# Performance work log

Hardware: AMD Instinct MI355X
Metric: run time of the kernel (lower is better)

Reference implementation:

```python
import jax, jax.numpy as jnp
import numpy as np

N_NODES = 100000
N_EDGES = 1600000
IN_C, HID_C, OUT_C = 128, 256, 256


def sage_conv(x, src, dst, W_l, b_l, W_r, n_nodes):
    # mean aggregation of source-node features onto destination nodes
    msg_sum = jax.ops.segment_sum(x[src], dst, num_segments=n_nodes)  # [N, F]
    deg = jax.ops.segment_sum(jnp.ones_like(dst, dtype=x.dtype), dst, num_segments=n_nodes)
    aggr = msg_sum / jnp.maximum(deg, 1.0)[:, None]
    # PyG SAGEConv: lin_l(aggr) (with bias) + lin_r(x) (no bias)
    return aggr @ W_l + b_l + x @ W_r


def setup_inputs() -> dict:
    key = jax.random.key(0)
    ks = jax.random.split(key, 12)
    x = jax.random.normal(ks[0], (N_NODES, IN_C), dtype=jnp.float32)
    edge_src = jax.random.randint(ks[1], (N_EDGES,), 0, N_NODES)
    edge_dst = jax.random.randint(ks[2], (N_EDGES,), 0, N_NODES)

    def glorot(k, fan_in, fan_out):
        s = jnp.sqrt(2.0 / (fan_in + fan_out)).astype(jnp.float32)
        return jax.random.normal(k, (fan_in, fan_out), dtype=jnp.float32) * s

    return {
        "x": x,
        "W_l0": glorot(ks[3], IN_C, HID_C), "b_l0": jnp.zeros((HID_C,), jnp.float32),
        "W_r0": glorot(ks[4], IN_C, HID_C),
        "W_l1": glorot(ks[5], HID_C, HID_C), "b_l1": jnp.zeros((HID_C,), jnp.float32),
        "W_r1": glorot(ks[6], HID_C, HID_C),
        "W_l2": glorot(ks[7], HID_C, OUT_C), "b_l2": jnp.zeros((OUT_C,), jnp.float32),
        "W_r2": glorot(ks[8], HID_C, OUT_C),
        "edge_src": edge_src,
        "edge_dst": edge_dst,
    }


def reference(x, W_l0, b_l0, W_r0, W_l1, b_l1, W_r1, W_l2, b_l2, W_r2, edge_src, edge_dst):
    n = x.shape[0]
    h = sage_conv(x, edge_src, edge_dst, W_l0, b_l0, W_r0, n)
    h = jax.nn.relu(h)  # dropout p=0.0 -> identity
    h = sage_conv(h, edge_src, edge_dst, W_l1, b_l1, W_r1, n)
    h = jax.nn.relu(h)
    h = sage_conv(h, edge_src, edge_dst, W_l2, b_l2, W_r2, n)
    return h
```

## Files before the change

### kernel.cpp

```cpp
#include <hip/hip_runtime.h>
#include <cstdint>
#include <cstddef>


#define N_NODES 100000
#define N_EDGES 1600000

#define SCAN_BLOCKS 256
#define SCAN_T 256
#define FILL_PASSES 4

typedef unsigned short ushort;
typedef unsigned int uint;
typedef __attribute__((ext_vector_type(8))) short short8;
typedef __attribute__((ext_vector_type(4))) float floatx4;

#define AS1 __attribute__((address_space(1)))
#define AS3 __attribute__((address_space(3)))

__device__ __forceinline__ float bf2f(ushort h) {
    union { uint u; float f; } c; c.u = ((uint)h) << 16; return c.f;
}
__device__ __forceinline__ ushort f2bf(float f) {
    union { float f; uint u; } c; c.f = f;
    uint u = c.u;
    return (ushort)((u + 0x7FFFu + ((u >> 16) & 1u)) >> 16);
}


__global__ void count_edges(const int* __restrict__ dst, int* __restrict__ cnt) {
    int i = blockIdx.x * blockDim.x + threadIdx.x;
    if (i < N_EDGES) atomicAdd(&cnt[dst[i]], 1);
}

__global__ __launch_bounds__(SCAN_T) void scan_partial(
    const int* __restrict__ cnt, int* __restrict__ bsum, int n)
{
    int chunk = (n + SCAN_BLOCKS - 1) / SCAN_BLOCKS;
    int beg = blockIdx.x * chunk;
    int end = beg + chunk; if (end > n) end = n;
    int t = threadIdx.x;
    int s = 0;
    for (int i = beg + t; i < end; i += SCAN_T) s += cnt[i];
    __shared__ int sh[SCAN_T];
    sh[t] = s;
    __syncthreads();
    for (int off = SCAN_T / 2; off > 0; off >>= 1) {
        if (t < off) sh[t] += sh[t + off];
        __syncthreads();
    }
    if (t == 0) bsum[blockIdx.x] = sh[0];
}

__global__ __launch_bounds__(SCAN_T) void scan_block_sums(int* __restrict__ bsum) {
    int t = threadIdx.x;
    __shared__ int sh[SCAN_T];
    int v = bsum[t];
    sh[t] = v;
    __syncthreads();
    for (int off = 1; off < SCAN_T; off <<= 1) {
        int u = (t >= off) ? sh[t - off] : 0;
        __syncthreads();
        sh[t] += u;
        __syncthreads();
    }
    bsum[t] = sh[t] - v;
}

__global__ __launch_bounds__(SCAN_T) void scan_fill(
    int* __restrict__ cnt, const int* __restrict__ bsum,
    int* __restrict__ row_ptr, int n)
{
    int chunk = (n + SCAN_BLOCKS - 1) / SCAN_BLOCKS;
    int beg = blockIdx.x * chunk;
    int end = beg + chunk; if (end > n) end = n;
    int t = threadIdx.x;
    int per = (chunk + SCAN_T - 1) / SCAN_T;
    int tb = beg + t * per;
    int te = tb + per; if (te > end) te = end;
    int s = 0;
    for (int i = tb; i < te; ++i) s += cnt[i];
    __shared__ int sh[SCAN_T];
    sh[t] = s;
    __syncthreads();
    for (int off = 1; off < SCAN_T; off <<= 1) {
        int u = (t >= off) ? sh[t - off] : 0;
        __syncthreads();
        sh[t] += u;
        __syncthreads();
    }
    int running = bsum[blockIdx.x] + sh[t] - s;
    for (int i = tb; i < te; ++i) {
        int c = cnt[i];
        row_ptr[i] = running;
        cnt[i] = running;
        running += c;
    }
    if (blockIdx.x == 0 && t == 0) row_ptr[n] = N_EDGES;
}

__global__ void fill_csr(const int* __restrict__ src, const int* __restrict__ dst,
                         int* __restrict__ cursor, int* __restrict__ col_idx) {
    int i = blockIdx.x * blockDim.x + threadIdx.x;
    if (i >= N_EDGES) return;
    int lo = (int)blockIdx.y * (N_NODES / FILL_PASSES);
    int hi = lo + (N_NODES / FILL_PASSES);
    int d = dst[i];
    if (d >= lo && d < hi) {
        int p = atomicAdd(&cursor[d], 1);
        col_idx[p] = src[i];
    }
}


__global__ void convert_x_bf16(const float* __restrict__ x, ushort* __restrict__ xb, int n4) {
    int i = blockIdx.x * blockDim.x + threadIdx.x;
    if (i >= n4) return;
    float4 v = *(const float4*)&x[(size_t)i * 4];
    ushort4 o;
    o.x = f2bf(v.x); o.y = f2bf(v.y); o.z = f2bf(v.z); o.w = f2bf(v.w);
    *(ushort4*)&xb[(size_t)i * 4] = o;
}

__global__ void transpose_w_bf16(const float* __restrict__ W, ushort* __restrict__ Wt, int kshift) {
    int i = blockIdx.x * blockDim.x + threadIdx.x;
    int K = 1 << kshift;
    if (i >= 256 * K) return;
    int n = i >> kshift;
    int k = i & (K - 1);
    Wt[i] = f2bf(W[k * 256 + n]);
}

__global__ __launch_bounds__(64) void aggregate_bf16(
    const ushort* __restrict__ xb, const int* __restrict__ row_ptr,
    const int* __restrict__ col_idx, ushort* __restrict__ outb, int F)
{
    int node = blockIdx.x;
    int t = threadIdx.x;
    int b = row_ptr[node], e = row_ptr[node + 1];
    float d = (float)(e - b); if (d < 1.f) d = 1.f;
    float inv = 1.f / d;

    if (F == 256) {
        int c = t * 4;
        float a0 = 0.f, a1 = 0.f, a2 = 0.f, a3 = 0.f;
        float b0 = 0.f, b1 = 0.f, b2 = 0.f, b3 = 0.f;
        int i = b;
        for (; i + 1 < e; i += 2) {
            int s0 = col_idx[i];
            int s1 = col_idx[i + 1];
            uint2 v0 = *(const uint2*)&xb[(size_t)s0 * 256 + c];
            uint2 v1 = *(const uint2*)&xb[(size_t)s1 * 256 + c];
            a0 += bf2f((ushort)(v0.x & 0xffff)); a1 += bf2f((ushort)(v0.x >> 16));
            a2 += bf2f((ushort)(v0.y & 0xffff)); a3 += bf2f((ushort)(v0.y >> 16));
            b0 += bf2f((ushort)(v1.x & 0xffff)); b1 += bf2f((ushort)(v1.x >> 16));
            b2 += bf2f((ushort)(v1.y & 0xffff)); b3 += bf2f((ushort)(v1.y >> 16));
        }
        if (i < e) {
            int s0 = col_idx[i];
            uint2 v0 = *(const uint2*)&xb[(size_t)s0 * 256 + c];
            a0 += bf2f((ushort)(v0.x & 0xffff)); a1 += bf2f((ushort)(v0.x >> 16));
            a2 += bf2f((ushort)(v0.y & 0xffff)); a3 += bf2f((ushort)(v0.y >> 16));
        }
        ushort4 o;
        o.x = f2bf((a0 + b0) * inv); o.y = f2bf((a1 + b1) * inv);
        o.z = f2bf((a2 + b2) * inv); o.w = f2bf((a3 + b3) * inv);
        *(ushort4*)&outb[(size_t)node * 256 + c] = o;
    } else {
        int c = t * 2;
        float a0 = 0.f, a1 = 0.f, b0 = 0.f, b1 = 0.f;
        int i = b;
        for (; i + 1 < e; i += 2) {
            int s0 = col_idx[i];
            int s1 = col_idx[i + 1];
            uint v0 = *(const uint*)&xb[(size_t)s0 * 128 + c];
            uint v1 = *(const uint*)&xb[(size_t)s1 * 128 + c];
            a0 += bf2f((ushort)(v0 & 0xffff)); a1 += bf2f((ushort)(v0 >> 16));
            b0 += bf2f((ushort)(v1 & 0xffff)); b1 += bf2f((ushort)(v1 >> 16));
        }
        if (i < e) {
            int s0 = col_idx[i];
            uint v0 = *(const uint*)&xb[(size_t)s0 * 128 + c];
            a0 += bf2f((ushort)(v0 & 0xffff)); a1 += bf2f((ushort)(v0 >> 16));
        }
        ushort2 o;
        o.x = f2bf((a0 + b0) * inv); o.y = f2bf((a1 + b1) * inv);
        *(ushort2*)&outb[(size_t)node * 128 + c] = o;
    }
}

__global__ __launch_bounds__(512, 4) void gemm_wres(
    const ushort* __restrict__ A1, const ushort* __restrict__ W1t,
    const ushort* __restrict__ A2, const ushort* __restrict__ W2t,
    const float* __restrict__ bias, ushort* __restrict__ out_bf,
    float* __restrict__ out_f32, int M, int K, int relu)
{
    __shared__ __align__(16) ushort Wl[32 * 128 * 8];
    int tid = threadIdx.x;
    int w = tid >> 6, lane = tid & 63;
    int m_ = lane & 15, koq = lane >> 4;
    int c0 = blockIdx.y * 128;
    int row0 = blockIdx.x * 256;
    int KQ = K >> 3;
    int nj = (KQ * 128) >> 9;
    int nk = K >> 5;

    floatx4 acc[2][8];
#pragma unroll
    for (int i = 0; i < 2; ++i)
#pragma unroll
        for (int f = 0; f < 8; ++f) acc[i][f] = (floatx4){0.f, 0.f, 0.f, 0.f};

    int ra = row0 + w * 32 + m_;      if (ra > M - 1) ra = M - 1;
    int rb = row0 + w * 32 + 16 + m_; if (rb > M - 1) rb = M - 1;

    for (int mm = 0; mm < 2; ++mm) {
        const ushort* __restrict__ A  = mm ? A2 : A1;
        const ushort* __restrict__ Wt = mm ? W2t : W1t;
        if (mm) __syncthreads();
        for (int j = 0; j < nj; ++j) {
            int s = j * 512 + tid;
            int q = s >> 7, col = s & 127;
            __builtin_amdgcn_global_load_lds(
                (const AS1 uint*)&Wt[(size_t)(c0 + col) * K + q * 8],
                (AS3 uint*)&Wl[(size_t)(j * 512 + w * 64) * 8], 16, 0, 0);
        }
        __syncthreads();

        const ushort* __restrict__ Aa = &A[(size_t)ra * K + koq * 8];
        const ushort* __restrict__ Ab = &A[(size_t)rb * K + koq * 8];

        short8 a0 = *(const short8*)&Aa[0];
        short8 a1 = *(const short8*)&Ab[0];
        for (int kk = 0; kk < nk; ++kk) {
            short8 n0, n1;
            if (kk + 1 < nk) {
                n0 = *(const short8*)&Aa[(kk + 1) * 32];
                n1 = *(const short8*)&Ab[(kk + 1) * 32];
            }
            const ushort* bbase = &Wl[(size_t)((kk * 4 + koq) * 128 + m_) * 8];
#pragma unroll
            for (int fc = 0; fc < 8; ++fc) {
                short8 b = *(const short8*)&bbase[fc * 128];
                acc[0][fc] = __builtin_amdgcn_mfma_f32_16x16x32_bf16(a0, b, acc[0][fc], 0, 0, 0);
                acc[1][fc] = __builtin_amdgcn_mfma_f32_16x16x32_bf16(a1, b, acc[1][fc], 0, 0, 0);
            }
            a0 = n0; a1 = n1;
        }
    }

#pragma unroll
    for (int m2 = 0; m2 < 2; ++m2) {
#pragma unroll
        for (int fc = 0; fc < 8; ++fc) {
            int col = c0 + fc * 16 + m_;
            float bv = bias[col];
#pragma unroll
            for (int r = 0; r < 4; ++r) {
                int row = row0 + w * 32 + m2 * 16 + koq * 4 + r;
                if (row >= M) continue;
                float v = acc[m2][fc][r] + bv;
                if (relu) v = fmaxf(v, 0.f);
                if (out_f32) out_f32[(size_t)row * 256 + col] = v;
                else         out_bf [(size_t)row * 256 + col] = f2bf(v);
            }
        }
    }
}


extern "C" void kernel_launch(void* const* d_in, const int* in_sizes, int n_in,
                              void* d_out, int out_size, void* d_ws, size_t ws_size,
                              hipStream_t stream) {
    const float* x    = (const float*)d_in[0];
    const float* W_l0 = (const float*)d_in[1];
    const float* b_l0 = (const float*)d_in[2];
    const float* W_r0 = (const float*)d_in[3];
    const float* W_l1 = (const float*)d_in[4];
    const float* b_l1 = (const float*)d_in[5];
    const float* W_r1 = (const float*)d_in[6];
    const float* W_l2 = (const float*)d_in[7];
    const float* b_l2 = (const float*)d_in[8];
    const float* W_r2 = (const float*)d_in[9];
    const int* esrc   = (const int*)d_in[10];
    const int* edst   = (const int*)d_in[11];
    float* out = (float*)d_out;

    size_t off = 0;
    char* ws = (char*)d_ws;
    auto take = [&](size_t bytes) -> void* {
        void* p = ws + off;
        off += (bytes + 255) & ~(size_t)255;
        return p;
    };
    int*    cnt     = (int*)take((size_t)N_NODES * 4);
    int*    row_ptr = (int*)take((size_t)(N_NODES + 1) * 4);
    int*    col_idx = (int*)take((size_t)N_EDGES * 4);
    int*    bsum    = (int*)take((size_t)SCAN_BLOCKS * 4);
    ushort* xb      = (ushort*)take((size_t)N_NODES * 128 * 2);
    ushort* Wl0t    = (ushort*)take((size_t)256 * 128 * 2);
    ushort* Wr0t    = (ushort*)take((size_t)256 * 128 * 2);
    ushort* Wl1t    = (ushort*)take((size_t)256 * 256 * 2);
    ushort* Wr1t    = (ushort*)take((size_t)256 * 256 * 2);
    ushort* Wl2t    = (ushort*)take((size_t)256 * 256 * 2);
    ushort* Wr2t    = (ushort*)take((size_t)256 * 256 * 2);
    ushort* aggrb   = (ushort*)take((size_t)N_NODES * 256 * 2);
    ushort* ha      = (ushort*)take((size_t)N_NODES * 256 * 2);
    ushort* hb      = (ushort*)take((size_t)N_NODES * 256 * 2);
    (void)ws_size; (void)in_sizes; (void)n_in; (void)out_size;

    hipMemsetAsync(cnt, 0, (size_t)N_NODES * 4, stream);
    int eb = (N_EDGES + 255) / 256;
    count_edges<<<eb, 256, 0, stream>>>(edst, cnt);
    scan_partial<<<SCAN_BLOCKS, SCAN_T, 0, stream>>>(cnt, bsum, N_NODES);
    scan_block_sums<<<1, SCAN_T, 0, stream>>>(bsum);
    scan_fill<<<SCAN_BLOCKS, SCAN_T, 0, stream>>>(cnt, bsum, row_ptr, N_NODES);
    fill_csr<<<dim3(eb, FILL_PASSES), 256, 0, stream>>>(esrc, edst, cnt, col_idx);

    int n4 = (N_NODES * 128) / 4;
    convert_x_bf16<<<(n4 + 255) / 256, 256, 0, stream>>>(x, xb, n4);
    transpose_w_bf16<<<(256 * 128 + 255) / 256, 256, 0, stream>>>(W_l0, Wl0t, 7);
    transpose_w_bf16<<<(256 * 128 + 255) / 256, 256, 0, stream>>>(W_r0, Wr0t, 7);
    transpose_w_bf16<<<(256 * 256 + 255) / 256, 256, 0, stream>>>(W_l1, Wl1t, 8);
    transpose_w_bf16<<<(256 * 256 + 255) / 256, 256, 0, stream>>>(W_r1, Wr1t, 8);
    transpose_w_bf16<<<(256 * 256 + 255) / 256, 256, 0, stream>>>(W_l2, Wl2t, 8);
    transpose_w_bf16<<<(256 * 256 + 255) / 256, 256, 0, stream>>>(W_r2, Wr2t, 8);

    dim3 ggrid((N_NODES + 255) / 256, 2);

    aggregate_bf16<<<N_NODES, 64, 0, stream>>>(xb, row_ptr, col_idx, aggrb, 128);
    gemm_wres<<<ggrid, 512, 0, stream>>>(aggrb, Wl0t, xb, Wr0t, b_l0,
                                         ha, nullptr, N_NODES, 128, 1);
    aggregate_bf16<<<N_NODES, 64, 0, stream>>>(ha, row_ptr, col_idx, aggrb, 256);
    gemm_wres<<<ggrid, 512, 0, stream>>>(aggrb, Wl1t, ha, Wr1t, b_l1,
                                         hb, nullptr, N_NODES, 256, 1);
    aggregate_bf16<<<N_NODES, 64, 0, stream>>>(hb, row_ptr, col_idx, aggrb, 256);
    gemm_wres<<<ggrid, 512, 0, stream>>>(aggrb, Wl2t, hb, Wr2t, b_l2,
                                         nullptr, out, N_NODES, 256, 0);
}
```

Before: 807.8 us.

## Fuse prep kernels and restructure GEMM into double-buffered K-chunked full-width tiles

```diff
diff --git a/kernel.cpp b/kernel.cpp
--- a/kernel.cpp
+++ b/kernel.cpp
@@ -28,10 +28,45 @@
 }
 
 
-__global__ void count_edges(const int* __restrict__ dst, int* __restrict__ cnt) {
+#define N4X (N_NODES * 128 / 4)
+
+__global__ void prep_all(
+    const int* __restrict__ dst, int* __restrict__ cnt,
+    const float* __restrict__ x, ushort* __restrict__ xb,
+    const float* __restrict__ Wl0, ushort* __restrict__ Wl0t,
+    const float* __restrict__ Wr0, ushort* __restrict__ Wr0t,
+    const float* __restrict__ Wl1, ushort* __restrict__ Wl1t,
+    const float* __restrict__ Wr1, ushort* __restrict__ Wr1t,
+    const float* __restrict__ Wl2, ushort* __restrict__ Wl2t,
+    const float* __restrict__ Wr2, ushort* __restrict__ Wr2t)
+{
     int i = blockIdx.x * blockDim.x + threadIdx.x;
-    if (i < N_EDGES) atomicAdd(&cnt[dst[i]], 1);
-}
+    if (i < N_EDGES) { atomicAdd(&cnt[dst[i]], 1); return; }
+    i -= N_EDGES;
+    if (i < N4X) {
+        float4 v = *(const float4*)&x[(size_t)i * 4];
+        ushort4 o;
+        o.x = f2bf(v.x); o.y = f2bf(v.y); o.z = f2bf(v.z); o.w = f2bf(v.w);
+        *(ushort4*)&xb[(size_t)i * 4] = o;
+        return;
+    }
+    i -= N4X;
+#define WT2(Wsrc, Wdst, LIM) \
+    if (i < (LIM)) { \
+        int q = i >> 11, col = (i >> 3) & 255, e = i & 7; \
+        Wdst[i] = f2bf(Wsrc[(q * 8 + e) * 256 + col]); \
+        return; \
+    } \
+    i -= (LIM);
+    WT2(Wl0, Wl0t, 32768)
+    WT2(Wr0, Wr0t, 32768)
+    WT2(Wl1, Wl1t, 65536)
+    WT2(Wr1, Wr1t, 65536)
+    WT2(Wl2, Wl2t, 65536)
+    WT2(Wr2, Wr2t, 65536)
+#undef WT2
+}
+
 
 __global__ __launch_bounds__(SCAN_T) void scan_partial(
     const int* __restrict__ cnt, int* __restrict__ bsum, int n)
@@ -110,25 +145,6 @@
         int p = atomicAdd(&cursor[d], 1);
         col_idx[p] = src[i];
     }
-}
-
-
-__global__ void convert_x_bf16(const float* __restrict__ x, ushort* __restrict__ xb, int n4) {
-    int i = blockIdx.x * blockDim.x + threadIdx.x;
-    if (i >= n4) return;
-    float4 v = *(const float4*)&x[(size_t)i * 4];
-    ushort4 o;
-    o.x = f2bf(v.x); o.y = f2bf(v.y); o.z = f2bf(v.z); o.w = f2bf(v.w);
-    *(ushort4*)&xb[(size_t)i * 4] = o;
-}
-
-__global__ void transpose_w_bf16(const float* __restrict__ W, ushort* __restrict__ Wt, int kshift) {
-    int i = blockIdx.x * blockDim.x + threadIdx.x;
-    int K = 1 << kshift;
-    if (i >= 256 * K) return;
-    int n = i >> kshift;
-    int k = i & (K - 1);
-    Wt[i] = f2bf(W[k * 256 + n]);
 }
 
 __global__ __launch_bounds__(64) void aggregate_bf16(
@@ -189,71 +205,85 @@
     }
 }
 
-__global__ __launch_bounds__(512, 4) void gemm_wres(
+__global__ __launch_bounds__(256, 2) void gemm_kc(
     const ushort* __restrict__ A1, const ushort* __restrict__ W1t,
     const ushort* __restrict__ A2, const ushort* __restrict__ W2t,
     const float* __restrict__ bias, ushort* __restrict__ out_bf,
     float* __restrict__ out_f32, int M, int K, int relu)
 {
-    __shared__ __align__(16) ushort Wl[32 * 128 * 8];
+    __shared__ __align__(16) ushort Wl[2][2048 * 8];
     int tid = threadIdx.x;
     int w = tid >> 6, lane = tid & 63;
     int m_ = lane & 15, koq = lane >> 4;
-    int c0 = blockIdx.y * 128;
-    int row0 = blockIdx.x * 256;
-    int KQ = K >> 3;
-    int nj = (KQ * 128) >> 9;
-    int nk = K >> 5;
-
-    floatx4 acc[2][8];
+    int row0 = blockIdx.x * 128;
+    int nc = K >> 6;
+
+    floatx4 acc[2][16];
 #pragma unroll
     for (int i = 0; i < 2; ++i)
 #pragma unroll
-        for (int f = 0; f < 8; ++f) acc[i][f] = (floatx4){0.f, 0.f, 0.f, 0.f};
+        for (int f = 0; f < 16; ++f) acc[i][f] = (floatx4){0.f, 0.f, 0.f, 0.f};
 
     int ra = row0 + w * 32 + m_;      if (ra > M - 1) ra = M - 1;
     int rb = row0 + w * 32 + 16 + m_; if (rb > M - 1) rb = M - 1;
+
+#define STAGE(c, buf) \
+    { \
+        const ushort* _s = &Wt[(size_t)(c) * 16384 + tid * 8]; \
+        _Pragma("unroll") \
+        for (int j = 0; j < 8; ++j) { \
+            __builtin_amdgcn_global_load_lds( \
+                (const AS1 uint*)&_s[(size_t)j * 2048], \
+                (AS3 uint*)&Wl[buf][(j * 256 + w * 64) * 8], 16, 0, 0); \
+        } \
+    }
 
     for (int mm = 0; mm < 2; ++mm) {
         const ushort* __restrict__ A  = mm ? A2 : A1;
         const ushort* __restrict__ Wt = mm ? W2t : W1t;
-        if (mm) __syncthreads();
-        for (int j = 0; j < nj; ++j) {
-            int s = j * 512 + tid;
-            int q = s >> 7, col = s & 127;
-            __builtin_amdgcn_global_load_lds(
-                (const AS1 uint*)&Wt[(size_t)(c0 + col) * K + q * 8],
-                (AS3 uint*)&Wl[(size_t)(j * 512 + w * 64) * 8], 16, 0, 0);
-        }
-        __syncthreads();
-
         const ushort* __restrict__ Aa = &A[(size_t)ra * K + koq * 8];
         const ushort* __restrict__ Ab = &A[(size_t)rb * K + koq * 8];
 
+        STAGE(0, 0)
         short8 a0 = *(const short8*)&Aa[0];
         short8 a1 = *(const short8*)&Ab[0];
-        for (int kk = 0; kk < nk; ++kk) {
-            short8 n0, n1;
-            if (kk + 1 < nk) {
-                n0 = *(const short8*)&Aa[(kk + 1) * 32];
-                n1 = *(const short8*)&Ab[(kk + 1) * 32];
+        short8 a2 = *(const short8*)&Aa[32];
+        short8 a3 = *(const short8*)&Ab[32];
+        __syncthreads();
+
+        for (int c = 0; c < nc; ++c) {
+            short8 n0, n1, n2, n3;
+            if (c + 1 < nc) {
+                STAGE(c + 1, (c + 1) & 1)
+                n0 = *(const short8*)&Aa[(c + 1) * 64];
+                n1 = *(const short8*)&Ab[(c + 1) * 64];
+                n2 = *(const short8*)&Aa[(c + 1) * 64 + 32];
+                n3 = *(const short8*)&Ab[(c + 1) * 64 + 32];
             }
-            const ushort* bbase = &Wl[(size_t)((kk * 4 + koq) * 128 + m_) * 8];
-#pragma unroll
-            for (int fc = 0; fc < 8; ++fc) {
-                short8 b = *(const short8*)&bbase[fc * 128];
-                acc[0][fc] = __builtin_amdgcn_mfma_f32_16x16x32_bf16(a0, b, acc[0][fc], 0, 0, 0);
-                acc[1][fc] = __builtin_amdgcn_mfma_f32_16x16x32_bf16(a1, b, acc[1][fc], 0, 0, 0);
+            int buf = c & 1;
+#pragma unroll
+            for (int kk = 0; kk < 2; ++kk) {
+                const ushort* bb = &Wl[buf][((kk * 4 + koq) * 256 + m_) * 8];
+                short8 aA = kk ? a2 : a0;
+                short8 aB = kk ? a3 : a1;
+#pragma unroll
+                for (int fc = 0; fc < 16; ++fc) {
+                    short8 b = *(const short8*)&bb[fc * 128];
+                    acc[0][fc] = __builtin_amdgcn_mfma_f32_16x16x32_bf16(aA, b, acc[0][fc], 0, 0, 0);
+                    acc[1][fc] = __builtin_amdgcn_mfma_f32_16x16x32_bf16(aB, b, acc[1][fc], 0, 0, 0);
+                }
             }
-            a0 = n0; a1 = n1;
-        }
-    }
+            __syncthreads();
+            a0 = n0; a1 = n1; a2 = n2; a3 = n3;
+        }
+    }
+#undef STAGE
 
 #pragma unroll
     for (int m2 = 0; m2 < 2; ++m2) {
 #pragma unroll
-        for (int fc = 0; fc < 8; ++fc) {
-            int col = c0 + fc * 16 + m_;
+        for (int fc = 0; fc < 16; ++fc) {
+            int col = fc * 16 + m_;
             float bv = bias[col];
 #pragma unroll
             for (int r = 0; r < 4; ++r) {
@@ -310,31 +340,26 @@
     (void)ws_size; (void)in_sizes; (void)n_in; (void)out_size;
 
     hipMemsetAsync(cnt, 0, (size_t)N_NODES * 4, stream);
-    int eb = (N_EDGES + 255) / 256;
-    count_edges<<<eb, 256, 0, stream>>>(edst, cnt);
+    int total_prep = N_EDGES + N4X + 2 * 32768 + 4 * 65536;
+    prep_all<<<(total_prep + 255) / 256, 256, 0, stream>>>(
+        edst, cnt, x, xb,
+        W_l0, Wl0t, W_r0, Wr0t, W_l1, Wl1t, W_r1, Wr1t, W_l2, Wl2t, W_r2, Wr2t);
+
     scan_partial<<<SCAN_BLOCKS, SCAN_T, 0, stream>>>(cnt, bsum, N_NODES);
     scan_block_sums<<<1, SCAN_T, 0, stream>>>(bsum);
     scan_fill<<<SCAN_BLOCKS, SCAN_T, 0, stream>>>(cnt, bsum, row_ptr, N_NODES);
+    int eb = (N_EDGES + 255) / 256;
     fill_csr<<<dim3(eb, FILL_PASSES), 256, 0, stream>>>(esrc, edst, cnt, col_idx);
 
-    int n4 = (N_NODES * 128) / 4;
-    convert_x_bf16<<<(n4 + 255) / 256, 256, 0, stream>>>(x, xb, n4);
-    transpose_w_bf16<<<(256 * 128 + 255) / 256, 256, 0, stream>>>(W_l0, Wl0t, 7);
-    transpose_w_bf16<<<(256 * 128 + 255) / 256, 256, 0, stream>>>(W_r0, Wr0t, 7);
-    transpose_w_bf16<<<(256 * 256 + 255) / 256, 256, 0, stream>>>(W_l1, Wl1t, 8);
-    transpose_w_bf16<<<(256 * 256 + 255) / 256, 256, 0, stream>>>(W_r1, Wr1t, 8);
-    transpose_w_bf16<<<(256 * 256 + 255) / 256, 256, 0, stream>>>(W_l2, Wl2t, 8);
-    transpose_w_bf16<<<(256 * 256 + 255) / 256, 256, 0, stream>>>(W_r2, Wr2t, 8);
-
-    dim3 ggrid((N_NODES + 255) / 256, 2);
+    dim3 ggrid((N_NODES + 127) / 128, 1);
 
     aggregate_bf16<<<N_NODES, 64, 0, stream>>>(xb, row_ptr, col_idx, aggrb, 128);
-    gemm_wres<<<ggrid, 512, 0, stream>>>(aggrb, Wl0t, xb, Wr0t, b_l0,
-                                         ha, nullptr, N_NODES, 128, 1);
+    gemm_kc<<<ggrid, 256, 0, stream>>>(aggrb, Wl0t, xb, Wr0t, b_l0,
+                                       ha, nullptr, N_NODES, 128, 1);
     aggregate_bf16<<<N_NODES, 64, 0, stream>>>(ha, row_ptr, col_idx, aggrb, 256);
-    gemm_wres<<<ggrid, 512, 0, stream>>>(aggrb, Wl1t, ha, Wr1t, b_l1,
-                                         hb, nullptr, N_NODES, 256, 1);
+    gemm_kc<<<ggrid, 256, 0, stream>>>(aggrb, Wl1t, ha, Wr1t, b_l1,
+                                       hb, nullptr, N_NODES, 256, 1);
     aggregate_bf16<<<N_NODES, 64, 0, stream>>>(hb, row_ptr, col_idx, aggrb, 256);
-    gemm_wres<<<ggrid, 512, 0, stream>>>(aggrb, Wl2t, hb, Wr2t, b_l2,
-                                         nullptr, out, N_NODES, 256, 0);
-}
+    gemm_kc<<<ggrid, 256, 0, stream>>>(aggrb, Wl2t, hb, Wr2t, b_l2,
+                                       nullptr, out, N_NODES, 256, 0);
+}
```

Result: no change. 808.9 us (+0.1%).
